# Optimization experiments

Measured on AMD Instinct MI355X. Metric: run time of the kernel, lower is better.

Reference implementation:

```python
import jax, jax.numpy as jnp
import numpy as np


def _sage_layer(h_src, src, dst, n_dst, Wself, Wneigh, b):
    # DGL SAGEConv('mean'): out = fc_self(h_dst) + fc_neigh(mean_{u->v} h_src[u]) + bias
    msg = jax.ops.segment_sum(h_src[src], dst, num_segments=n_dst)          # [n_dst, d]
    deg = jax.ops.segment_sum(jnp.ones(src.shape, h_src.dtype), dst, num_segments=n_dst)
    mean = msg / jnp.maximum(deg, 1.0)[:, None]
    h_dst = h_src[:n_dst]  # DGL block convention: dst nodes are first n_dst src nodes
    return h_dst @ Wself.T + mean @ Wneigh.T + b


def setup_inputs() -> dict:
    key = jax.random.key(0)
    ks = jax.random.split(key, 12)
    d_in, d_h, d_out = 128, 128, 64
    N0, N1, N2, N3 = 500000, 100000, 20000, 5000
    E0, E1, E2 = 2000000, 400000, 100000
    s = 0.05
    return {
        "input_feats": jax.random.normal(ks[0], (N0, d_in), jnp.float32),
        "src0": jax.random.randint(ks[1], (E0,), 0, N0),
        "dst0": jax.random.randint(ks[2], (E0,), 0, N1),
        "src1": jax.random.randint(ks[3], (E1,), 0, N1),
        "dst1": jax.random.randint(ks[4], (E1,), 0, N2),
        "src2": jax.random.randint(ks[5], (E2,), 0, N2),
        "dst2": jax.random.randint(ks[6], (E2,), 0, N3),
        "n_dst0": N1, "n_dst1": N2, "n_dst2": N3,
        "Wself0": jax.random.normal(ks[7], (d_h, d_in), jnp.float32) * s,
        "Wneigh0": jax.random.normal(ks[8], (d_h, d_in), jnp.float32) * s,
        "b0": jnp.zeros((d_h,), jnp.float32),
        "Wself1": jax.random.normal(ks[9], (d_h, d_h), jnp.float32) * s,
        "Wneigh1": jax.random.normal(ks[10], (d_h, d_h), jnp.float32) * s,
        "b1": jnp.zeros((d_h,), jnp.float32),
        "Wself2": jax.random.normal(ks[11], (d_out, d_h), jnp.float32) * s,
        "Wneigh2": jax.random.normal(jax.random.fold_in(key, 99), (d_out, d_h), jnp.float32) * s,
        "b2": jnp.zeros((d_out,), jnp.float32),
    }


def reference(input_feats, src0, dst0, src1, dst1, src2, dst2,
              n_dst0, n_dst1, n_dst2,
              Wself0, Wneigh0, b0, Wself1, Wneigh1, b1, Wself2, Wneigh2, b2):
    # Layer 0 (+ FeatureShuffle == identity on a single device) + relu (dropout=0)
    h = _sage_layer(input_feats, src0, dst0, n_dst0, Wself0, Wneigh0, b0)
    h = jax.nn.relu(h)
    # Layer 1 + relu
    h = _sage_layer(h, src1, dst1, n_dst1, Wself1, Wneigh1, b1)
    h = jax.nn.relu(h)
    # Layer 2 (output, no activation)
    h = _sage_layer(h, src2, dst2, n_dst2, Wself2, Wneigh2, b2)
    return h
```

## Files before the change

### kernel.cpp

```cpp
#include <hip/hip_runtime.h>

#define K_DIM 128
#define NTOT   125000
#define RPB    512
#define NB     245

typedef __attribute__((ext_vector_type(8))) short bf16x8;
typedef __attribute__((ext_vector_type(8))) unsigned short u16x8;
typedef __attribute__((ext_vector_type(4))) float f32x4;

static __device__ __forceinline__ unsigned short f2bf(float f) {
    union { float f; unsigned u; } v; v.f = f;
    unsigned r = v.u + 0x7FFF + ((v.u >> 16) & 1);
    return (unsigned short)(r >> 16);
}
static __device__ __forceinline__ float bf2f(unsigned short b) {
    union { unsigned u; float f; } v; v.u = ((unsigned)b) << 16;
    return v.f;
}

__global__ __launch_bounds__(256)
void prep_kernel(const float* __restrict__ feats, unsigned short* __restrict__ feats_bf,
                 int nchunk, int CFB,
                 const float* __restrict__ w0s, const float* __restrict__ w0n,
                 const float* __restrict__ w1s, const float* __restrict__ w1n,
                 const float* __restrict__ w2s, const float* __restrict__ w2n,
                 unsigned short* __restrict__ wbf,
                 const int* __restrict__ d0, const int* __restrict__ d1,
                 const int* __restrict__ d2, int E0, int E1, int Etot,
                 int* __restrict__ bucket_cnt)
{
    __shared__ int hist[256];
    int b = blockIdx.x;
    int t = threadIdx.x;

    if (b < CFB) {
        int stride = CFB * 256;
        for (int i = b * 256 + t; i < nchunk; i += stride) {
            float4 a = reinterpret_cast<const float4*>(feats)[2 * (long)i];
            float4 c = reinterpret_cast<const float4*>(feats)[2 * (long)i + 1];
            uint4 o;
            o.x = (unsigned)f2bf(a.x) | ((unsigned)f2bf(a.y) << 16);
            o.y = (unsigned)f2bf(a.z) | ((unsigned)f2bf(a.w) << 16);
            o.z = (unsigned)f2bf(c.x) | ((unsigned)f2bf(c.y) << 16);
            o.w = (unsigned)f2bf(c.z) | ((unsigned)f2bf(c.w) << 16);
            reinterpret_cast<uint4*>(feats_bf)[i] = o;
        }
    } else if (b < CFB + 320) {
        int idx = (b - CFB) * 256 + t;
        if (idx >= 81920) return;
        if (idx < 16384) {
            wbf[idx] = f2bf(w0s[idx]);
        } else if (idx < 32768) {
            int i = idx - 16384; float v = w0n[i];
            unsigned short hi = f2bf(v);
            wbf[16384 + i] = hi;
            wbf[32768 + i] = f2bf(v - bf2f(hi));
        } else if (idx < 49152) {
            int i = idx - 32768;
            wbf[49152 + i] = f2bf(w1s[i]);
        } else if (idx < 65536) {
            int i = idx - 49152; float v = w1n[i];
            unsigned short hi = f2bf(v);
            wbf[65536 + i] = hi;
            wbf[81920 + i] = f2bf(v - bf2f(hi));
        } else if (idx < 73728) {
            int i = idx - 65536;
            wbf[98304 + i] = f2bf(w2s[i]);
        } else {
            int i = idx - 73728; float v = w2n[i];
            unsigned short hi = f2bf(v);
            wbf[106496 + i] = hi;
            wbf[114688 + i] = f2bf(v - bf2f(hi));
        }
    } else {
        hist[t] = 0;
        __syncthreads();
        int cb = b - CFB - 320;
        int stride = 512 * 256;
        for (int e = cb * 256 + t; e < Etot; e += stride) {
            int row;
            if (e < E0)           row = d0[e];
            else if (e < E0 + E1) row = 100000 + d1[e - E0];
            else                  row = 120000 + d2[e - E0 - E1];
            atomicAdd(&hist[row >> 9], 1);
        }
        __syncthreads();
        if (t < NB && hist[t]) atomicAdd(&bucket_cnt[t], hist[t]);
    }
}

static __device__ __forceinline__ void edge_decode(
    int e,
    const int* __restrict__ s0, const int* __restrict__ d0,
    const int* __restrict__ s1, const int* __restrict__ d1,
    const int* __restrict__ s2, const int* __restrict__ d2,
    int E0, int E1, int& row, int& src)
{
    if (e < E0)           { row = d0[e];                    src = s0[e]; }
    else if (e < E0 + E1) { row = 100000 + d1[e - E0];      src = s1[e - E0]; }
    else                  { row = 120000 + d2[e - E0 - E1]; src = s2[e - E0 - E1]; }
}

__global__ __launch_bounds__(256)
void bucket_scan_kernel(const int* __restrict__ bucket_cnt,
                        int* __restrict__ bucket_base,
                        int* __restrict__ bucket_cursor, int Etot)
{
    __shared__ int sm[256];
    int t = threadIdx.x;
    int v = (t < NB) ? bucket_cnt[t] : 0;
    sm[t] = v;
    __syncthreads();
    for (int s = 1; s < 256; s <<= 1) {
        int a = (t >= s) ? sm[t - s] : 0;
        __syncthreads();
        sm[t] += a;
        __syncthreads();
    }
    int excl = sm[t] - v;
    if (t < NB) { bucket_base[t] = excl; bucket_cursor[t] = excl; }
    if (t == 0) bucket_base[NB] = Etot;
}

#define CHUNK 4096
__global__ __launch_bounds__(256)
void bucket_scatter_kernel(const int* __restrict__ s0, const int* __restrict__ d0,
                           const int* __restrict__ s1, const int* __restrict__ d1,
                           const int* __restrict__ s2, const int* __restrict__ d2,
                           int E0, int E1, int Etot,
                           int* __restrict__ bucket_cursor,
                           int2* __restrict__ ebuf)
{
    __shared__ int hist[256];
    __shared__ int start[256];
    int t = threadIdx.x;
    int base = blockIdx.x * CHUNK;
    hist[t] = 0;
    __syncthreads();

    #pragma unroll
    for (int i = 0; i < CHUNK / 256; ++i) {
        int e = base + i * 256 + t;
        if (e < Etot) {
            int row;
            if (e < E0)           row = d0[e];
            else if (e < E0 + E1) row = 100000 + d1[e - E0];
            else                  row = 120000 + d2[e - E0 - E1];
            atomicAdd(&hist[row >> 9], 1);
        }
    }
    __syncthreads();
    if (t < NB) {
        int c = hist[t];
        start[t] = c ? atomicAdd(&bucket_cursor[t], c) : 0;
    }
    __syncthreads();
    hist[t] = 0;
    __syncthreads();

    #pragma unroll
    for (int i = 0; i < CHUNK / 256; ++i) {
        int e = base + i * 256 + t;
        if (e < Etot) {
            int row, src;
            edge_decode(e, s0, d0, s1, d1, s2, d2, E0, E1, row, src);
            int b = row >> 9;
            int pos = start[b] + atomicAdd(&hist[b], 1);
            ebuf[pos] = make_int2(row, src);
        }
    }
}

__global__ __launch_bounds__(256)
void bucket_fill_kernel(const int2* __restrict__ ebuf,
                        const int* __restrict__ bucket_base,
                        int* __restrict__ rowstart,
                        int* __restrict__ csr, int Etot)
{
    __shared__ int hist[RPB];
    __shared__ int ps[256];
    __shared__ int rst[RPB];

    int t = threadIdx.x;
    int b = blockIdx.x;
    int e0 = bucket_base[b], e1 = bucket_base[b + 1];
    int row0 = b << 9;
    int nrows = min(RPB, NTOT - row0);

    hist[t] = 0; hist[t + 256] = 0;
    __syncthreads();
    for (int e = e0 + t; e < e1; e += 256)
        atomicAdd(&hist[ebuf[e].x - row0], 1);
    __syncthreads();

    int a0 = hist[2 * t], a1 = hist[2 * t + 1];
    int pv = a0 + a1;
    ps[t] = pv;
    __syncthreads();
    for (int s = 1; s < 256; s <<= 1) {
        int a = (t >= s) ? ps[t - s] : 0;
        __syncthreads();
        ps[t] += a;
        __syncthreads();
    }
    int pe = ps[t] - pv;
    rst[2 * t] = pe;
    rst[2 * t + 1] = pe + a0;
    __syncthreads();

    if (2 * t < nrows)     rowstart[row0 + 2 * t]     = e0 + rst[2 * t];
    if (2 * t + 1 < nrows) rowstart[row0 + 2 * t + 1] = e0 + rst[2 * t + 1];
    if (b == NB - 1 && t == 0) rowstart[NTOT] = Etot;
    hist[2 * t] = rst[2 * t];
    hist[2 * t + 1] = rst[2 * t + 1];
    __syncthreads();

    for (int e = e0 + t; e < e1; e += 256) {
        int2 p = ebuf[e];
        int off = atomicAdd(&hist[p.x - row0], 1);
        csr[e0 + off] = p.y;
    }
}

__global__ __launch_bounds__(256)
void gather_mean_f32_kernel(const float* __restrict__ h,
                            const int* __restrict__ csr,
                            const int* __restrict__ rs,
                            unsigned short* __restrict__ msgb, int n)
{
    long gid = (long)blockIdx.x * 256 + threadIdx.x;
    int g = (int)(gid >> 5);
    int lane = (int)(gid & 31);
    if (g >= n) return;

    int s0 = rs[g], s1 = rs[g + 1];
    float4 acc = make_float4(0.f, 0.f, 0.f, 0.f);
    int e = s0;
    for (; e + 4 <= s1; e += 4) {
        int i0 = csr[e], i1 = csr[e + 1], i2 = csr[e + 2], i3 = csr[e + 3];
        float4 v0 = reinterpret_cast<const float4*>(h + (long)i0 * K_DIM)[lane];
        float4 v1 = reinterpret_cast<const float4*>(h + (long)i1 * K_DIM)[lane];
        float4 v2 = reinterpret_cast<const float4*>(h + (long)i2 * K_DIM)[lane];
        float4 v3 = reinterpret_cast<const float4*>(h + (long)i3 * K_DIM)[lane];
        acc.x += (v0.x + v1.x) + (v2.x + v3.x);
        acc.y += (v0.y + v1.y) + (v2.y + v3.y);
        acc.z += (v0.z + v1.z) + (v2.z + v3.z);
        acc.w += (v0.w + v1.w) + (v2.w + v3.w);
    }
    for (; e < s1; ++e) {
        int i0 = csr[e];
        float4 v0 = reinterpret_cast<const float4*>(h + (long)i0 * K_DIM)[lane];
        acc.x += v0.x; acc.y += v0.y; acc.z += v0.z; acc.w += v0.w;
    }
    float rd = 1.0f / fmaxf((float)(s1 - s0), 1.0f);
    ushort4 o;
    o.x = f2bf(acc.x * rd); o.y = f2bf(acc.y * rd);
    o.z = f2bf(acc.z * rd); o.w = f2bf(acc.w * rd);
    reinterpret_cast<ushort4*>(msgb + (long)g * K_DIM)[lane] = o;
}

__global__ __launch_bounds__(256)
void gather_mean_bf_kernel(const unsigned short* __restrict__ hb,
                           const int* __restrict__ csr,
                           const int* __restrict__ rs,
                           unsigned short* __restrict__ msgb, int n)
{
    long gid = (long)blockIdx.x * 256 + threadIdx.x;
    int g = (int)(gid >> 4);
    int lane = (int)(gid & 15);
    if (g >= n) return;

    int s0 = rs[g], s1 = rs[g + 1];
    float a[8] = {0.f, 0.f, 0.f, 0.f, 0.f, 0.f, 0.f, 0.f};
    const unsigned short* hb_l = hb + lane * 8;

    int e = s0;
    for (; e + 8 <= s1; e += 8) {
        int idx[8];
        #pragma unroll
        for (int i = 0; i < 8; ++i) idx[i] = csr[e + i];
        #pragma unroll
        for (int i = 0; i < 8; ++i) {
            u16x8 v = *reinterpret_cast<const u16x8*>(hb_l + (long)idx[i] * K_DIM);
            #pragma unroll
            for (int j = 0; j < 8; ++j) a[j] += bf2f(v[j]);
        }
    }
    for (; e < s1; ++e) {
        u16x8 v = *reinterpret_cast<const u16x8*>(hb_l + (long)csr[e] * K_DIM);
        #pragma unroll
        for (int j = 0; j < 8; ++j) a[j] += bf2f(v[j]);
    }
    float rd = 1.0f / fmaxf((float)(s1 - s0), 1.0f);
    u16x8 o;
    #pragma unroll
    for (int j = 0; j < 8; ++j) o[j] = f2bf(a[j] * rd);
    *reinterpret_cast<u16x8*>(msgb + (long)g * K_DIM + lane * 8) = o;
}

template<int NCOL, bool RELU, bool WRITE_BF>
__global__ __launch_bounds__(256, 3)
void sage_gemm_mfma(const float* __restrict__ h,
                    const unsigned short* __restrict__ msgb,
                    const unsigned short* __restrict__ wsb,
                    const unsigned short* __restrict__ wnh,
                    const unsigned short* __restrict__ wnl,
                    const float* __restrict__ bias,
                    float* __restrict__ out,
                    unsigned short* __restrict__ outb,
                    int n)
{
    constexpr int NCB = NCOL / 16;
    __shared__ bf16x8 Ah[8][64];
    __shared__ bf16x8 Al[8][64];
    __shared__ bf16x8 Ms[8][64];
    __shared__ bf16x8 Bs[NCB][64];
    __shared__ bf16x8 Bh[NCB][64];
    __shared__ bf16x8 Bl[NCB][64];

    const int t    = threadIdx.x;
    const int lane = t & 63;
    const int w    = t >> 6;
    const int row0 = blockIdx.x * 128;

    f32x4 acc[2][NCB];
    #pragma unroll
    for (int rf = 0; rf < 2; ++rf)
        #pragma unroll
        for (int cb = 0; cb < NCB; ++cb)
            acc[rf][cb] = (f32x4){0.f, 0.f, 0.f, 0.f};

    const int arow   = t & 127;
    const int ah2    = t >> 7;
    const int grow_a = min(row0 + arow, n - 1);
    const int arb    = arow >> 4;

    for (int kc = 0; kc < 128; kc += 32) {
        __syncthreads();
        #pragma unroll
        for (int i = 0; i < 2; ++i) {
            int hh = ah2 * 2 + i;
            const float* src = h + (long)grow_a * 128 + kc + hh * 8;
            float4 x = *reinterpret_cast<const float4*>(src);
            float4 y = *reinterpret_cast<const float4*>(src + 4);
            float xs[8] = {x.x, x.y, x.z, x.w, y.x, y.y, y.z, y.w};
            bf16x8 hi8, lo8;
            #pragma unroll
            for (int j = 0; j < 8; ++j) {
                unsigned short hu = f2bf(xs[j]);
                hi8[j] = (short)hu;
                lo8[j] = (short)f2bf(xs[j] - bf2f(hu));
            }
            int li = hh * 16 + (arow & 15);
            Ah[arb][li] = hi8;
            Al[arb][li] = lo8;
            Ms[arb][li] = *reinterpret_cast<const bf16x8*>(
                              msgb + (long)grow_a * 128 + kc + hh * 8);
        }
        if (NCOL == 128) {
            int col = t & 127, h2 = t >> 7;
            #pragma unroll
            for (int i = 0; i < 2; ++i) {
                int hh = h2 * 2 + i;
                int li = hh * 16 + (col & 15);
                int cb = col >> 4;
                long o = (long)col * 128 + kc + hh * 8;
                Bs[cb][li] = *reinterpret_cast<const bf16x8*>(wsb + o);
                Bh[cb][li] = *reinterpret_cast<const bf16x8*>(wnh + o);
                Bl[cb][li] = *reinterpret_cast<const bf16x8*>(wnl + o);
            }
        } else {
            int col = t & 63, hh = t >> 6;
            int li = hh * 16 + (col & 15);
            int cb = col >> 4;
            long o = (long)col * 128 + kc + hh * 8;
            Bs[cb][li] = *reinterpret_cast<const bf16x8*>(wsb + o);
            Bh[cb][li] = *reinterpret_cast<const bf16x8*>(wnh + o);
            Bl[cb][li] = *reinterpret_cast<const bf16x8*>(wnl + o);
        }
        __syncthreads();

        bf16x8 a0h = Ah[2 * w][lane],     a0l = Al[2 * w][lane],     m0 = Ms[2 * w][lane];
        bf16x8 a1h = Ah[2 * w + 1][lane], a1l = Al[2 * w + 1][lane], m1 = Ms[2 * w + 1][lane];
        #pragma unroll
        for (int cb = 0; cb < NCB; ++cb) {
            bf16x8 bs = Bs[cb][lane];
            bf16x8 bh = Bh[cb][lane];
            bf16x8 bl = Bl[cb][lane];
            acc[0][cb] = __builtin_amdgcn_mfma_f32_16x16x32_bf16(a0h, bs, acc[0][cb], 0, 0, 0);
            acc[0][cb] = __builtin_amdgcn_mfma_f32_16x16x32_bf16(a0l, bs, acc[0][cb], 0, 0, 0);
            acc[0][cb] = __builtin_amdgcn_mfma_f32_16x16x32_bf16(m0,  bh, acc[0][cb], 0, 0, 0);
            acc[0][cb] = __builtin_amdgcn_mfma_f32_16x16x32_bf16(m0,  bl, acc[0][cb], 0, 0, 0);
            acc[1][cb] = __builtin_amdgcn_mfma_f32_16x16x32_bf16(a1h, bs, acc[1][cb], 0, 0, 0);
            acc[1][cb] = __builtin_amdgcn_mfma_f32_16x16x32_bf16(a1l, bs, acc[1][cb], 0, 0, 0);
            acc[1][cb] = __builtin_amdgcn_mfma_f32_16x16x32_bf16(m1,  bh, acc[1][cb], 0, 0, 0);
            acc[1][cb] = __builtin_amdgcn_mfma_f32_16x16x32_bf16(m1,  bl, acc[1][cb], 0, 0, 0);
        }
    }

    #pragma unroll
    for (int rf = 0; rf < 2; ++rf) {
        #pragma unroll
        for (int cb = 0; cb < NCB; ++cb) {
            int col = cb * 16 + (lane & 15);
            float bv = bias[col];
            #pragma unroll
            for (int r = 0; r < 4; ++r) {
                int grow = row0 + w * 32 + rf * 16 + (lane >> 4) * 4 + r;
                if (grow < n) {
                    float v = acc[rf][cb][r] + bv;
                    if (RELU) v = fmaxf(v, 0.f);
                    out[(long)grow * NCOL + col] = v;
                    if (WRITE_BF) outb[(long)grow * NCOL + col] = f2bf(v);
                }
            }
        }
    }
}

extern "C" void kernel_launch(void* const* d_in, const int* in_sizes, int n_in,
                              void* d_out, int out_size, void* d_ws, size_t ws_size,
                              hipStream_t stream)
{
    const float* feats   = (const float*)d_in[0];
    const int*   src0    = (const int*)d_in[1];
    const int*   dst0    = (const int*)d_in[2];
    const int*   src1    = (const int*)d_in[3];
    const int*   dst1    = (const int*)d_in[4];
    const int*   src2    = (const int*)d_in[5];
    const int*   dst2    = (const int*)d_in[6];
    const float* Wself0  = (const float*)d_in[10];
    const float* Wneigh0 = (const float*)d_in[11];
    const float* b0      = (const float*)d_in[12];
    const float* Wself1  = (const float*)d_in[13];
    const float* Wneigh1 = (const float*)d_in[14];
    const float* b1      = (const float*)d_in[15];
    const float* Wself2  = (const float*)d_in[16];
    const float* Wneigh2 = (const float*)d_in[17];
    const float* b2      = (const float*)d_in[18];

    const int E0 = in_sizes[1];
    const int E1 = in_sizes[3];
    const int E2 = in_sizes[5];
    const int Etot = E0 + E1 + E2;
    const int N1 = 100000, N2 = 20000, N3 = 5000;

    char* base = (char*)d_ws;
    const bool bfp = ws_size >= 164500000ull;

    unsigned short* feats_bf; float* h1; unsigned short* h1b;
    float* h2; unsigned short* h2b;
    unsigned short* msgb; int2* ebuf; int* csr; int* rowstart;
    int* bcnt; int* bbase; int* bcur; unsigned short* wbf;

    if (bfp) {
        feats_bf = (unsigned short*)base;
        h1   = (float*)base;
        h1b  = (unsigned short*)(base + 51200000);
        h2   = (float*)(base + 76800000);
        h2b  = (unsigned short*)(base + 87040000);
        msgb = (unsigned short*)(base + 128000000);
        csr      = (int*)(base + 153600000);
        rowstart = (int*)(base + 163600000);
        bcnt     = (int*)(base + 164100224);
        bbase    = bcnt + 256;
        bcur     = bbase + 256;
        wbf      = (unsigned short*)(base + 164103296);
    } else {
        feats_bf = nullptr;
        h1   = (float*)base;
        h1b  = nullptr;
        h2   = (float*)(base + 51200000);
        h2b  = nullptr;
        msgb = (unsigned short*)(base + 61440000);
        csr      = (int*)(base + 87040000);
        rowstart = (int*)(base + 97040000);
        bcnt     = (int*)(base + 97540224);
        bbase    = bcnt + 256;
        bcur     = bbase + 256;
        wbf      = (unsigned short*)(base + 97543296);
    }
    ebuf = (int2*)msgb;

    const int CFB = bfp ? 2048 : 0;
    hipMemsetAsync(bcnt, 0, 1024, stream);
    prep_kernel<<<CFB + 320 + 512, 256, 0, stream>>>(
        feats, feats_bf, bfp ? 8000000 : 0, CFB,
        Wself0, Wneigh0, Wself1, Wneigh1, Wself2, Wneigh2, wbf,
        dst0, dst1, dst2, E0, E1, Etot, bcnt);
    bucket_scan_kernel<<<1, 256, 0, stream>>>(bcnt, bbase, bcur, Etot);
    bucket_scatter_kernel<<<(Etot + CHUNK - 1) / CHUNK, 256, 0, stream>>>(
        src0, dst0, src1, dst1, src2, dst2, E0, E1, Etot, bcur, ebuf);
    bucket_fill_kernel<<<NB, 256, 0, stream>>>(ebuf, bbase, rowstart, csr, Etot);

    if (bfp) {
        gather_mean_bf_kernel<<<(N1 * 16 + 255) / 256, 256, 0, stream>>>(
            feats_bf, csr, rowstart, msgb, N1);
        sage_gemm_mfma<128, true, true><<<(N1 + 127) / 128, 256, 0, stream>>>(
            feats, msgb, wbf, wbf + 16384, wbf + 32768, b0, h1, h1b, N1);
        gather_mean_bf_kernel<<<(N2 * 16 + 255) / 256, 256, 0, stream>>>(
            h1b, csr, rowstart + 100000, msgb, N2);
        sage_gemm_mfma<128, true, true><<<(N2 + 127) / 128, 256, 0, stream>>>(
            h1, msgb, wbf + 49152, wbf + 65536, wbf + 81920, b1, h2, h2b, N2);
        gather_mean_bf_kernel<<<(N3 * 16 + 255) / 256, 256, 0, stream>>>(
            h2b, csr, rowstart + 120000, msgb, N3);
        sage_gemm_mfma<64, false, false><<<(N3 + 127) / 128, 256, 0, stream>>>(
            h2, msgb, wbf + 98304, wbf + 106496, wbf + 114688, b2,
            (float*)d_out, nullptr, N3);
    } else {
        gather_mean_f32_kernel<<<(N1 * 32 + 255) / 256, 256, 0, stream>>>(
            feats, csr, rowstart, msgb, N1);
        sage_gemm_mfma<128, true, false><<<(N1 + 127) / 128, 256, 0, stream>>>(
            feats, msgb, wbf, wbf + 16384, wbf + 32768, b0, h1, nullptr, N1);
        gather_mean_f32_kernel<<<(N2 * 32 + 255) / 256, 256, 0, stream>>>(
            h1, csr, rowstart + 100000, msgb, N2);
        sage_gemm_mfma<128, true, false><<<(N2 + 127) / 128, 256, 0, stream>>>(
            h1, msgb, wbf + 49152, wbf + 65536, wbf + 81920, b1, h2, nullptr, N2);
        gather_mean_f32_kernel<<<(N3 * 32 + 255) / 256, 256, 0, stream>>>(
            h2, csr, rowstart + 120000, msgb, N3);
        sage_gemm_mfma<64, false, false><<<(N3 + 127) / 128, 256, 0, stream>>>(
            h2, msgb, wbf + 98304, wbf + 106496, wbf + 114688, b2,
            (float*)d_out, nullptr, N3);
    }
}
```

Measured before the change: 356.8 us.

## Overlap feature bf16 conversion with CSR build and pack edge buffer

Moves the input-feature fp32-to-bf16 conversion out of the prep kernel and splits it into halves. Each half runs in extra blocks of the scatter and fill kernels, so the bandwidth-bound conversion can overlap the latency-bound bucket sort. The edge buffer now packs the local row and the source into one 32-bit int instead of an int2, halving its traffic. In the bf16 path, the GEMM skips fp32 stores for rows the next layer never reads as fp32, since only the first n_dst of the next layer are needed. The packing assumes source ids fit in 19 bits.

```diff
diff --git a/kernel.cpp b/kernel.cpp
--- a/kernel.cpp
+++ b/kernel.cpp
@@ -4,6 +4,8 @@
 #define NTOT   125000
 #define RPB    512
 #define NB     245
+#define SRC_BITS 19
+#define SRC_MASK 0x7FFFF
 
 typedef __attribute__((ext_vector_type(8))) short bf16x8;
 typedef __attribute__((ext_vector_type(8))) unsigned short u16x8;
@@ -19,35 +21,51 @@
     return v.f;
 }
 
+static __device__ __forceinline__ void conv_feat_part(
+    const float* __restrict__ feats, unsigned short* __restrict__ feats_bf,
+    int c0, int c1, int b0, int ncb, int b, int t)
+{
+    int stride = ncb * 256;
+    for (long i = c0 + (long)(b - b0) * 256 + t; i < c1; i += stride) {
+        float4 a = reinterpret_cast<const float4*>(feats)[2 * i];
+        float4 c = reinterpret_cast<const float4*>(feats)[2 * i + 1];
+        uint4 o;
+        o.x = (unsigned)f2bf(a.x) | ((unsigned)f2bf(a.y) << 16);
+        o.y = (unsigned)f2bf(a.z) | ((unsigned)f2bf(a.w) << 16);
+        o.z = (unsigned)f2bf(c.x) | ((unsigned)f2bf(c.y) << 16);
+        o.w = (unsigned)f2bf(c.z) | ((unsigned)f2bf(c.w) << 16);
+        reinterpret_cast<uint4*>(feats_bf)[i] = o;
+    }
+}
+
 __global__ __launch_bounds__(256)
-void prep_kernel(const float* __restrict__ feats, unsigned short* __restrict__ feats_bf,
-                 int nchunk, int CFB,
-                 const float* __restrict__ w0s, const float* __restrict__ w0n,
-                 const float* __restrict__ w1s, const float* __restrict__ w1n,
-                 const float* __restrict__ w2s, const float* __restrict__ w2n,
-                 unsigned short* __restrict__ wbf,
-                 const int* __restrict__ d0, const int* __restrict__ d1,
-                 const int* __restrict__ d2, int E0, int E1, int Etot,
-                 int* __restrict__ bucket_cnt)
+void prep1_kernel(const int* __restrict__ d0, const int* __restrict__ d1,
+                  const int* __restrict__ d2, int E0, int E1, int Etot,
+                  int* __restrict__ bucket_cnt,
+                  const float* __restrict__ w0s, const float* __restrict__ w0n,
+                  const float* __restrict__ w1s, const float* __restrict__ w1n,
+                  const float* __restrict__ w2s, const float* __restrict__ w2n,
+                  unsigned short* __restrict__ wbf)
 {
     __shared__ int hist[256];
     int b = blockIdx.x;
     int t = threadIdx.x;
 
-    if (b < CFB) {
-        int stride = CFB * 256;
-        for (int i = b * 256 + t; i < nchunk; i += stride) {
-            float4 a = reinterpret_cast<const float4*>(feats)[2 * (long)i];
-            float4 c = reinterpret_cast<const float4*>(feats)[2 * (long)i + 1];
-            uint4 o;
-            o.x = (unsigned)f2bf(a.x) | ((unsigned)f2bf(a.y) << 16);
-            o.y = (unsigned)f2bf(a.z) | ((unsigned)f2bf(a.w) << 16);
-            o.z = (unsigned)f2bf(c.x) | ((unsigned)f2bf(c.y) << 16);
-            o.w = (unsigned)f2bf(c.z) | ((unsigned)f2bf(c.w) << 16);
-            reinterpret_cast<uint4*>(feats_bf)[i] = o;
-        }
-    } else if (b < CFB + 320) {
-        int idx = (b - CFB) * 256 + t;
+    if (b < 512) {
+        hist[t] = 0;
+        __syncthreads();
+        int stride = 512 * 256;
+        for (int e = b * 256 + t; e < Etot; e += stride) {
+            int row;
+            if (e < E0)           row = d0[e];
+            else if (e < E0 + E1) row = 100000 + d1[e - E0];
+            else                  row = 120000 + d2[e - E0 - E1];
+            atomicAdd(&hist[row >> 9], 1);
+        }
+        __syncthreads();
+        if (t < NB && hist[t]) atomicAdd(&bucket_cnt[t], hist[t]);
+    } else {
+        int idx = (b - 512) * 256 + t;
         if (idx >= 81920) return;
         if (idx < 16384) {
             wbf[idx] = f2bf(w0s[idx]);
@@ -73,33 +91,7 @@
             wbf[106496 + i] = hi;
             wbf[114688 + i] = f2bf(v - bf2f(hi));
         }
-    } else {
-        hist[t] = 0;
-        __syncthreads();
-        int cb = b - CFB - 320;
-        int stride = 512 * 256;
-        for (int e = cb * 256 + t; e < Etot; e += stride) {
-            int row;
-            if (e < E0)           row = d0[e];
-            else if (e < E0 + E1) row = 100000 + d1[e - E0];
-            else                  row = 120000 + d2[e - E0 - E1];
-            atomicAdd(&hist[row >> 9], 1);
-        }
-        __syncthreads();
-        if (t < NB && hist[t]) atomicAdd(&bucket_cnt[t], hist[t]);
-    }
-}
-
-static __device__ __forceinline__ void edge_decode(
-    int e,
-    const int* __restrict__ s0, const int* __restrict__ d0,
-    const int* __restrict__ s1, const int* __restrict__ d1,
-    const int* __restrict__ s2, const int* __restrict__ d2,
-    int E0, int E1, int& row, int& src)
-{
-    if (e < E0)           { row = d0[e];                    src = s0[e]; }
-    else if (e < E0 + E1) { row = 100000 + d1[e - E0];      src = s1[e - E0]; }
-    else                  { row = 120000 + d2[e - E0 - E1]; src = s2[e - E0 - E1]; }
+    }
 }
 
 __global__ __launch_bounds__(256)
@@ -125,17 +117,27 @@
 
 #define CHUNK 4096
 __global__ __launch_bounds__(256)
-void bucket_scatter_kernel(const int* __restrict__ s0, const int* __restrict__ d0,
-                           const int* __restrict__ s1, const int* __restrict__ d1,
-                           const int* __restrict__ s2, const int* __restrict__ d2,
-                           int E0, int E1, int Etot,
-                           int* __restrict__ bucket_cursor,
-                           int2* __restrict__ ebuf)
+void scatter_conv_kernel(const int* __restrict__ s0, const int* __restrict__ d0,
+                         const int* __restrict__ s1, const int* __restrict__ d1,
+                         const int* __restrict__ s2, const int* __restrict__ d2,
+                         int E0, int E1, int Etot,
+                         int* __restrict__ bucket_cursor,
+                         int* __restrict__ ebuf,
+                         const float* __restrict__ feats,
+                         unsigned short* __restrict__ feats_bf,
+                         int cmid, int SCB, int ncb)
 {
     __shared__ int hist[256];
     __shared__ int start[256];
     int t = threadIdx.x;
-    int base = blockIdx.x * CHUNK;
+    int b = blockIdx.x;
+
+    if (b >= SCB) {
+        conv_feat_part(feats, feats_bf, 0, cmid, SCB, ncb, b, t);
+        return;
+    }
+
+    int base = b * CHUNK;
     hist[t] = 0;
     __syncthreads();
 
@@ -164,19 +166,24 @@
         int e = base + i * 256 + t;
         if (e < Etot) {
             int row, src;
-            edge_decode(e, s0, d0, s1, d1, s2, d2, E0, E1, row, src);
-            int b = row >> 9;
-            int pos = start[b] + atomicAdd(&hist[b], 1);
-            ebuf[pos] = make_int2(row, src);
+            if (e < E0)           { row = d0[e];                    src = s0[e]; }
+            else if (e < E0 + E1) { row = 100000 + d1[e - E0];      src = s1[e - E0]; }
+            else                  { row = 120000 + d2[e - E0 - E1]; src = s2[e - E0 - E1]; }
+            int bb = row >> 9;
+            int pos = start[bb] + atomicAdd(&hist[bb], 1);
+            ebuf[pos] = ((row & (RPB - 1)) << SRC_BITS) | src;
         }
     }
 }
 
 __global__ __launch_bounds__(256)
-void bucket_fill_kernel(const int2* __restrict__ ebuf,
-                        const int* __restrict__ bucket_base,
-                        int* __restrict__ rowstart,
-                        int* __restrict__ csr, int Etot)
+void fill_conv_kernel(const int* __restrict__ ebuf,
+                      const int* __restrict__ bucket_base,
+                      int* __restrict__ rowstart,
+                      int* __restrict__ csr, int Etot,
+                      const float* __restrict__ feats,
+                      unsigned short* __restrict__ feats_bf,
+                      int cmid, int ctot, int ncb)
 {
     __shared__ int hist[RPB];
     __shared__ int ps[256];
@@ -184,6 +191,12 @@
 
     int t = threadIdx.x;
     int b = blockIdx.x;
+
+    if (b >= NB) {
+        conv_feat_part(feats, feats_bf, cmid, ctot, NB, ncb, b, t);
+        return;
+    }
+
     int e0 = bucket_base[b], e1 = bucket_base[b + 1];
     int row0 = b << 9;
     int nrows = min(RPB, NTOT - row0);
@@ -191,7 +204,7 @@
     hist[t] = 0; hist[t + 256] = 0;
     __syncthreads();
     for (int e = e0 + t; e < e1; e += 256)
-        atomicAdd(&hist[ebuf[e].x - row0], 1);
+        atomicAdd(&hist[(unsigned)ebuf[e] >> SRC_BITS], 1);
     __syncthreads();
 
     int a0 = hist[2 * t], a1 = hist[2 * t + 1];
@@ -217,9 +230,9 @@
     __syncthreads();
 
     for (int e = e0 + t; e < e1; e += 256) {
-        int2 p = ebuf[e];
-        int off = atomicAdd(&hist[p.x - row0], 1);
-        csr[e0 + off] = p.y;
+        unsigned p = (unsigned)ebuf[e];
+        int off = atomicAdd(&hist[p >> SRC_BITS], 1);
+        csr[e0 + off] = p & SRC_MASK;
     }
 }
 
@@ -309,7 +322,7 @@
                     const float* __restrict__ bias,
                     float* __restrict__ out,
                     unsigned short* __restrict__ outb,
-                    int n)
+                    int n, int nf32)
 {
     constexpr int NCB = NCOL / 16;
     __shared__ bf16x8 Ah[8][64];
@@ -411,7 +424,7 @@
                 if (grow < n) {
                     float v = acc[rf][cb][r] + bv;
                     if (RELU) v = fmaxf(v, 0.f);
-                    out[(long)grow * NCOL + col] = v;
+                    if (grow < nf32) out[(long)grow * NCOL + col] = v;
                     if (WRITE_BF) outb[(long)grow * NCOL + col] = f2bf(v);
                 }
             }
@@ -451,7 +464,7 @@
 
     unsigned short* feats_bf; float* h1; unsigned short* h1b;
     float* h2; unsigned short* h2b;
-    unsigned short* msgb; int2* ebuf; int* csr; int* rowstart;
+    unsigned short* msgb; int* ebuf; int* csr; int* rowstart;
     int* bcnt; int* bbase; int* bcur; unsigned short* wbf;
 
     if (bfp) {
@@ -481,46 +494,51 @@
         bcur     = bbase + 256;
         wbf      = (unsigned short*)(base + 97543296);
     }
-    ebuf = (int2*)msgb;
-
-    const int CFB = bfp ? 2048 : 0;
+    ebuf = (int*)msgb;
+
+    const int SCB  = (Etot + CHUNK - 1) / CHUNK;
+    const int NCV  = bfp ? 1024 : 0;
+    const int CTOT = bfp ? 8000000 : 0;
+    const int CMID = CTOT / 2;
+
     hipMemsetAsync(bcnt, 0, 1024, stream);
-    prep_kernel<<<CFB + 320 + 512, 256, 0, stream>>>(
-        feats, feats_bf, bfp ? 8000000 : 0, CFB,
-        Wself0, Wneigh0, Wself1, Wneigh1, Wself2, Wneigh2, wbf,
-        dst0, dst1, dst2, E0, E1, Etot, bcnt);
+    prep1_kernel<<<832, 256, 0, stream>>>(
+        dst0, dst1, dst2, E0, E1, Etot, bcnt,
+        Wself0, Wneigh0, Wself1, Wneigh1, Wself2, Wneigh2, wbf);
     bucket_scan_kernel<<<1, 256, 0, stream>>>(bcnt, bbase, bcur, Etot);
-    bucket_scatter_kernel<<<(Etot + CHUNK - 1) / CHUNK, 256, 0, stream>>>(
-        src0, dst0, src1, dst1, src2, dst2, E0, E1, Etot, bcur, ebuf);
-    bucket_fill_kernel<<<NB, 256, 0, stream>>>(ebuf, bbase, rowstart, csr, Etot);
+    scatter_conv_kernel<<<SCB + NCV, 256, 0, stream>>>(
+        src0, dst0, src1, dst1, src2, dst2, E0, E1, Etot, bcur, ebuf,
+        feats, feats_bf, CMID, SCB, NCV);
+    fill_conv_kernel<<<NB + NCV, 256, 0, stream>>>(
+        ebuf, bbase, rowstart, csr, Etot, feats, feats_bf, CMID, CTOT, NCV);
 
     if (bfp) {
         gather_mean_bf_kernel<<<(N1 * 16 + 255) / 256, 256, 0, stream>>>(
             feats_bf, csr, rowstart, msgb, N1);
         sage_gemm_mfma<128, true, true><<<(N1 + 127) / 128, 256, 0, stream>>>(
-            feats, msgb, wbf, wbf + 16384, wbf + 32768, b0, h1, h1b, N1);
+            feats, msgb, wbf, wbf + 16384, wbf + 32768, b0, h1, h1b, N1, N2);
         gather_mean_bf_kernel<<<(N2 * 16 + 255) / 256, 256, 0, stream>>>(
             h1b, csr, rowstart + 100000, msgb, N2);
         sage_gemm_mfma<128, true, true><<<(N2 + 127) / 128, 256, 0, stream>>>(
-            h1, msgb, wbf + 49152, wbf + 65536, wbf + 81920, b1, h2, h2b, N2);
+            h1, msgb, wbf + 49152, wbf + 65536, wbf + 81920, b1, h2, h2b, N2, N3);
         gather_mean_bf_kernel<<<(N3 * 16 + 255) / 256, 256, 0, stream>>>(
             h2b, csr, rowstart + 120000, msgb, N3);
         sage_gemm_mfma<64, false, false><<<(N3 + 127) / 128, 256, 0, stream>>>(
             h2, msgb, wbf + 98304, wbf + 106496, wbf + 114688, b2,
-            (float*)d_out, nullptr, N3);
+            (float*)d_out, nullptr, N3, N3);
     } else {
         gather_mean_f32_kernel<<<(N1 * 32 + 255) / 256, 256, 0, stream>>>(
             feats, csr, rowstart, msgb, N1);
         sage_gemm_mfma<128, true, false><<<(N1 + 127) / 128, 256, 0, stream>>>(
-            feats, msgb, wbf, wbf + 16384, wbf + 32768, b0, h1, nullptr, N1);
+            feats, msgb, wbf, wbf + 16384, wbf + 32768, b0, h1, nullptr, N1, N1);
         gather_mean_f32_kernel<<<(N2 * 32 + 255) / 256, 256, 0, stream>>>(
             h1, csr, rowstart + 100000, msgb, N2);
         sage_gemm_mfma<128, true, false><<<(N2 + 127) / 128, 256, 0, stream>>>(
-            h1, msgb, wbf + 49152, wbf + 65536, wbf + 81920, b1, h2, nullptr, N2);
+            h1, msgb, wbf + 49152, wbf + 65536, wbf + 81920, b1, h2, nullptr, N2, N2);
         gather_mean_f32_kernel<<<(N3 * 32 + 255) / 256, 256, 0, stream>>>(
             h2, csr, rowstart + 120000, msgb, N3);
         sage_gemm_mfma<64, false, false><<<(N3 + 127) / 128, 256, 0, stream>>>(
             h2, msgb, wbf + 98304, wbf + 106496, wbf + 114688, b2,
-            (float*)d_out, nullptr, N3);
-    }
-}
+            (float*)d_out, nullptr, N3, N3);
+    }
+}
```

Measured after the change: 342.7 us. 4.0% less time.
